# Kernel optimization log

Hardware: AMD Instinct MI355X
Metric: run time of the kernel (lower is better)

## Reference

```python
import jax, jax.numpy as jnp
import numpy as np

DIM = 2048
HEADS = 16
DIM_HEAD = 128
DIM_INNER = HEADS * DIM_HEAD
BATCH = 2
SEQ = 2048
EPS = 1e-12  # F.normalize default eps


def l2norm(t, axis=-1):
    # matches F.normalize(t, dim=axis, p=2): t / max(||t||, eps)
    n = jnp.sqrt(jnp.sum(t * t, axis=axis, keepdims=True))
    return t / jnp.maximum(n, EPS)


def setup_inputs() -> dict:
    key = jax.random.key(0)
    ks = jax.random.split(key, 5)
    x = jax.random.normal(ks[0], (BATCH, SEQ, DIM), dtype=jnp.float32)
    # NormLinear weights (torch Linear layout: [out, in]); parametrization
    # l2-normalizes rows (dim=-1) for q/k/v and columns (dim=0) for to_out.
    Wq = jax.random.normal(ks[1], (DIM_INNER, DIM), dtype=jnp.float32) / np.sqrt(DIM)
    Wk = jax.random.normal(ks[2], (DIM_INNER, DIM), dtype=jnp.float32) / np.sqrt(DIM)
    Wv = jax.random.normal(ks[3], (DIM_INNER, DIM), dtype=jnp.float32) / np.sqrt(DIM)
    Wout = jax.random.normal(ks[4], (DIM, DIM_INNER), dtype=jnp.float32) / np.sqrt(DIM_INNER)
    # Scale(dim_inner, init=1.0, scale=dim**-1): param = ones * dim**-1,
    # forward_scale = init/scale = dim, so qk_scale() starts at 1.0
    qk_scale = jnp.ones((DIM_INNER,), dtype=jnp.float32) / DIM
    return {"x": x, "Wq": Wq, "Wk": Wk, "Wv": Wv, "Wout": Wout, "qk_scale": qk_scale}


def reference(x, Wq, Wk, Wv, Wout, qk_scale):
    b, n, _ = x.shape
    # NormLinear: x @ l2norm(W, rows).T  (scale = groups**-1 = 1)
    q = jnp.einsum('bnd,ed->bne', x, l2norm(Wq, axis=-1))
    k = jnp.einsum('bnd,ed->bne', x, l2norm(Wk, axis=-1))
    v = jnp.einsum('bnd,ed->bne', x, l2norm(Wv, axis=-1))
    # split heads: b n (h d) -> b h n d
    split = lambda t: t.reshape(b, n, HEADS, DIM_HEAD).transpose(0, 2, 1, 3)
    q, k, v = split(q), split(k), split(v)
    # per-head l2norm of q and k over head dim
    q = l2norm(q, axis=-1)
    k = l2norm(k, axis=-1)
    # learned qk scale: (h d) -> h 1 d, effective = param * forward_scale(=DIM)
    q = q * (qk_scale * DIM).reshape(HEADS, 1, DIM_HEAD)
    # causal SDPA with scale = sqrt(dim_head) (unit-norm q,k in nGPT)
    attn_scale = DIM_HEAD ** 0.5
    scores = jnp.einsum('bhid,bhjd->bhij', q, k) * attn_scale
    causal = jnp.tril(jnp.ones((n, n), dtype=bool))
    scores = jnp.where(causal, scores, jnp.finfo(scores.dtype).min)
    attn = jax.nn.softmax(scores, axis=-1)
    out = jnp.einsum('bhij,bhjd->bhid', attn, v)
    # merge heads: b h n d -> b n (h d)
    out = out.transpose(0, 2, 1, 3).reshape(b, n, DIM_INNER)
    # to_out: NormLinear with norm over dim=0 of weight [DIM, DIM_INNER]
    out = jnp.einsum('bne,de->bnd', out, l2norm(Wout, axis=0))
    return out
```

## Files before the change

### kernel.cpp

```cpp
#include <hip/hip_runtime.h>


typedef __bf16 bf16x8 __attribute__((ext_vector_type(8)));
typedef float f32x4 __attribute__((ext_vector_type(4)));

__device__ __forceinline__ unsigned short f2bf(float f) {
  unsigned int u = __float_as_uint(f);
  u = u + 0x7FFFu + ((u >> 16) & 1u);
  return (unsigned short)(u >> 16);
}

__device__ __forceinline__ void async16(const void* g, void* l) {
  __builtin_amdgcn_global_load_lds(
      (const __attribute__((address_space(1))) unsigned int*)g,
      (__attribute__((address_space(3))) unsigned int*)l, 16, 0, 0);
}

#define QFOLD (2048.0f * 11.313708498984761f * 1.4426950408889634f)

__global__ __launch_bounds__(256) void prep_all(
    const float* __restrict__ x, const float* __restrict__ Wq,
    const float* __restrict__ Wk, const float* __restrict__ Wv,
    const float* __restrict__ qks, ushort* __restrict__ xbf,
    ushort* __restrict__ wqn, ushort* __restrict__ wkn,
    ushort* __restrict__ wvn, float* __restrict__ colss,
    float* __restrict__ mh) {
  const int bid = blockIdx.x;
  const int t = threadIdx.x;
  if (bid < 6144) {
    const int z = bid >> 11, row = bid & 2047;
    const float* W = (z == 0) ? Wq : (z == 1) ? Wk : Wv;
    ushort* O = (z == 0) ? wqn : (z == 1) ? wkn : wvn;
    const float4* Wr = (const float4*)(W + (size_t)row * 2048);
    float4 v0 = Wr[t];
    float4 v1 = Wr[t + 256];
    float ss = v0.x * v0.x + v0.y * v0.y + v0.z * v0.z + v0.w * v0.w +
               v1.x * v1.x + v1.y * v1.y + v1.z * v1.z + v1.w * v1.w;
    ss += __shfl_xor(ss, 1);  ss += __shfl_xor(ss, 2);
    ss += __shfl_xor(ss, 4);  ss += __shfl_xor(ss, 8);
    ss += __shfl_xor(ss, 16); ss += __shfl_xor(ss, 32);
    __shared__ float red[4];
    if ((t & 63) == 0) red[t >> 6] = ss;
    __syncthreads();
    float tot = red[0] + red[1] + red[2] + red[3];
    float sc = 1.0f / fmaxf(sqrtf(tot), 1e-12f);
    ushort4 o0, o1;
    o0.x = f2bf(v0.x * sc); o0.y = f2bf(v0.y * sc);
    o0.z = f2bf(v0.z * sc); o0.w = f2bf(v0.w * sc);
    o1.x = f2bf(v1.x * sc); o1.y = f2bf(v1.y * sc);
    o1.z = f2bf(v1.z * sc); o1.w = f2bf(v1.w * sc);
    *(ushort4*)(O + (size_t)row * 2048 + t * 4) = o0;
    *(ushort4*)(O + (size_t)row * 2048 + 1024 + t * 4) = o1;
  } else if (bid < 14336) {
    const int idx = ((bid - 6144) * 256 + t) * 4;
    float4 v = *(const float4*)(x + idx);
    ushort4 o;
    o.x = f2bf(v.x); o.y = f2bf(v.y); o.z = f2bf(v.z); o.w = f2bf(v.w);
    *(ushort4*)(xbf + idx) = o;
  } else if (bid < 14352) {
    const int h = bid - 14336;
    if (t < 64) {
      const int l = t;
      float m = fmaxf(fabsf(qks[h * 128 + l]), fabsf(qks[h * 128 + 64 + l]));
      m = fmaxf(m, __shfl_xor(m, 1));  m = fmaxf(m, __shfl_xor(m, 2));
      m = fmaxf(m, __shfl_xor(m, 4));  m = fmaxf(m, __shfl_xor(m, 8));
      m = fmaxf(m, __shfl_xor(m, 16)); m = fmaxf(m, __shfl_xor(m, 32));
      if (l == 0) mh[h] = m * QFOLD;
    }
  } else {
    float4 z4 = (float4){0.f, 0.f, 0.f, 0.f};
    ((float4*)colss)[t] = z4;
    ((float4*)colss)[t + 256] = z4;
  }
}

__global__ __launch_bounds__(256) void wout_colss(const float* __restrict__ W,
                                                  float* __restrict__ colss) {
  const int e = blockIdx.x * 256 + threadIdx.x;
  const int d0 = blockIdx.y * 128;
  float ss = 0.f;
  #pragma unroll 8
  for (int i = 0; i < 128; ++i) {
    float v = W[(size_t)(d0 + i) * 2048 + e];
    ss += v * v;
  }
  atomicAdd(colss + e, ss);
}

__global__ __launch_bounds__(256) void wout_norm(const float* __restrict__ W,
                                                 const float* __restrict__ colss,
                                                 ushort* __restrict__ O) {
  const int idx = (blockIdx.x * 256 + threadIdx.x) * 4;
  float4 v = *(const float4*)(W + idx);
  float4 c = *(const float4*)(colss + (idx & 2047));
  ushort4 o;
  o.x = f2bf(v.x / fmaxf(sqrtf(c.x), 1e-12f));
  o.y = f2bf(v.y / fmaxf(sqrtf(c.y), 1e-12f));
  o.z = f2bf(v.z / fmaxf(sqrtf(c.z), 1e-12f));
  o.w = f2bf(v.w / fmaxf(sqrtf(c.w), 1e-12f));
  *(ushort4*)(O + idx) = o;
}

__global__ __launch_bounds__(256, 2) void gemm_qkv_fused(
    const ushort* __restrict__ X, const ushort* __restrict__ Wq,
    const ushort* __restrict__ Wk, const ushort* __restrict__ Wv,
    const float* __restrict__ qks, ushort* __restrict__ qn,
    ushort* __restrict__ kn, ushort* __restrict__ vt) {
  const int n0 = blockIdx.x * 128;
  const int m0 = blockIdx.y * 128;
  __shared__ __align__(16) char lds[4 * 16384];
  __shared__ float partials[2][128];
  const int t = threadIdx.x, w = t >> 6, l = t & 63;
  const int wm = w & 1, wn = w >> 1;
  const int l15 = l & 15, l4 = l >> 4;

  f32x4 acc[3][4][4];
  #pragma unroll
  for (int z = 0; z < 3; ++z)
    #pragma unroll
    for (int i = 0; i < 4; ++i)
      #pragma unroll
      for (int j = 0; j < 4; ++j) acc[z][i][j] = (f32x4){0.f, 0.f, 0.f, 0.f};

  const int lc = (t & 7) ^ ((t >> 3) & 7);
  const size_t soff = (size_t)(t >> 3) * 2048 + lc * 8;
  const ushort* sA = X + (size_t)m0 * 2048 + soff;
  const ushort* sQ = Wq + (size_t)n0 * 2048 + soff;
  const ushort* sK = Wk + (size_t)n0 * 2048 + soff;
  const ushort* sV = Wv + (size_t)n0 * 2048 + soff;
  char* dst = lds + t * 16;

  const int rdA = (wm * 64 + l15) * 128;
  const int rdB = (wn * 64 + l15) * 128;
  const int cb0 = (l4 ^ (l15 & 7)) * 16;
  const int cb1 = ((4 + l4) ^ (l15 & 7)) * 16;

  for (int kt = 0; kt < 32; ++kt) {
    const int k0 = kt * 64;
    __syncthreads();
    #pragma unroll
    for (int o = 0; o < 4; ++o) {
      async16(sA + o * 65536 + k0, dst + o * 4096);
      async16(sQ + o * 65536 + k0, dst + 16384 + o * 4096);
      async16(sK + o * 65536 + k0, dst + 32768 + o * 4096);
      async16(sV + o * 65536 + k0, dst + 49152 + o * 4096);
    }
    __syncthreads();
    #pragma unroll
    for (int ks = 0; ks < 2; ++ks) {
      const int cb = ks ? cb1 : cb0;
      bf16x8 af[4];
      #pragma unroll
      for (int f = 0; f < 4; ++f)
        af[f] = *(const bf16x8*)(lds + rdA + f * 2048 + cb);
      #pragma unroll
      for (int z = 0; z < 3; ++z) {
        const char* Bb = lds + 16384 * (1 + z);
        bf16x8 bg[4];
        #pragma unroll
        for (int f = 0; f < 4; ++f)
          bg[f] = *(const bf16x8*)(Bb + rdB + f * 2048 + cb);
        #pragma unroll
        for (int fm = 0; fm < 4; ++fm)
          #pragma unroll
          for (int fn = 0; fn < 4; ++fn)
            acc[z][fm][fn] = __builtin_amdgcn_mfma_f32_16x16x32_bf16(
                af[fm], bg[fn], acc[z][fm][fn], 0, 0, 0);
      }
    }
  }

  const int h = n0 >> 7;

  #pragma unroll
  for (int fm = 0; fm < 4; ++fm) {
    int mrow = m0 + wm * 64 + fm * 16 + l4 * 4;
    int bb = mrow >> 11;
    int nn = mrow & 2047;
    #pragma unroll
    for (int fn = 0; fn < 4; ++fn) {
      int d = wn * 64 + fn * 16 + l15;
      ushort4 p;
      p.x = f2bf(acc[2][fm][fn][0]); p.y = f2bf(acc[2][fm][fn][1]);
      p.z = f2bf(acc[2][fm][fn][2]); p.w = f2bf(acc[2][fm][fn][3]);
      *(ushort4*)(vt + (size_t)((bb * 16 + h) * 128 + d) * 2048 + nn) = p;
    }
  }

  #pragma unroll
  for (int z = 0; z < 2; ++z) {
    __syncthreads();
    float rs[4][4];
    #pragma unroll
    for (int fm = 0; fm < 4; ++fm)
      #pragma unroll
      for (int r = 0; r < 4; ++r) {
        float s = 0.f;
        #pragma unroll
        for (int fn = 0; fn < 4; ++fn) {
          float v = acc[z][fm][fn][r];
          s += v * v;
        }
        s += __shfl_xor(s, 1); s += __shfl_xor(s, 2);
        s += __shfl_xor(s, 4); s += __shfl_xor(s, 8);
        rs[fm][r] = s;
      }
    if (l15 == 0) {
      #pragma unroll
      for (int fm = 0; fm < 4; ++fm)
        #pragma unroll
        for (int r = 0; r < 4; ++r)
          partials[wn][wm * 64 + fm * 16 + l4 * 4 + r] = rs[fm][r];
    }
    __syncthreads();
    float cs[4];
    #pragma unroll
    for (int fn = 0; fn < 4; ++fn)
      cs[fn] = (z == 0) ? qks[n0 + wn * 64 + fn * 16 + l15] * QFOLD : 1.0f;
    ushort* O = (z == 0) ? qn : kn;
    #pragma unroll
    for (int fm = 0; fm < 4; ++fm)
      #pragma unroll
      for (int r = 0; r < 4; ++r) {
        int i = wm * 64 + fm * 16 + l4 * 4 + r;
        float tot = partials[0][i] + partials[1][i];
        float sc = 1.0f / fmaxf(sqrtf(tot), 1e-12f);
        #pragma unroll
        for (int fn = 0; fn < 4; ++fn)
          O[(size_t)(m0 + i) * 2048 + n0 + wn * 64 + fn * 16 + l15] =
              f2bf(acc[z][fm][fn][r] * sc * cs[fn]);
      }
  }
}


#define LDSBUF 49152
#define ABYTES 32768

__device__ __forceinline__ void mainloop_256x128(
    const ushort* __restrict__ A, const ushort* __restrict__ Bw,
    int m0, int n0, char* lds, f32x4 acc[4][4], int t) {
  const int l = t & 63, w = t >> 6;
  const int wm = w & 3, wn = w >> 2;
  const int l15 = l & 15, l4 = l >> 4;

  const int lc = (t & 7) ^ ((t >> 3) & 7);
  const ushort* srcA = A + (size_t)m0 * 2048 + (t >> 3) * 2048 + lc * 8;
  const ushort* srcB = Bw + (size_t)n0 * 2048 + (t >> 3) * 2048 + lc * 8;
  char* dstA = lds + t * 16;
  char* dstB = lds + ABYTES + t * 16;

  const int rdA = (wm * 64 + l15) * 128;
  const int rdB = ABYTES + (wn * 64 + l15) * 128;
  const int cb0 = ((l4 ^ (l15 & 7)) * 16);
  const int cb1 = (((4 + l4) ^ (l15 & 7)) * 16);

  auto stageA = [&](int s, int k0, int o) {
    async16(srcA + (size_t)o * 131072 + k0, dstA + s * LDSBUF + o * 8192);
  };
  auto stageB = [&](int s, int k0, int o) {
    async16(srcB + (size_t)o * 131072 + k0, dstB + s * LDSBUF + o * 8192);
  };

  #pragma unroll
  for (int i = 0; i < 4; ++i)
    #pragma unroll
    for (int j = 0; j < 4; ++j) acc[i][j] = (f32x4){0.f, 0.f, 0.f, 0.f};

  stageA(0, 0, 0); stageA(0, 0, 1); stageA(0, 0, 2); stageA(0, 0, 3);
  stageB(0, 0, 0); stageB(0, 0, 1);
  stageA(1, 64, 0); stageA(1, 64, 1); stageA(1, 64, 2); stageA(1, 64, 3);
  stageB(1, 64, 0); stageB(1, 64, 1);
  asm volatile("s_waitcnt vmcnt(6)" ::: "memory");
  __builtin_amdgcn_s_barrier();

  auto tile = [&](int s, int s2, int k2, bool pf) {
    const char* Ab = lds + s * LDSBUF;
    bf16x8 af[4][2], bg[4][2];
    #pragma unroll
    for (int fm = 0; fm < 4; ++fm) {
      af[fm][0] = *(const bf16x8*)(Ab + rdA + fm * 2048 + cb0);
      af[fm][1] = *(const bf16x8*)(Ab + rdA + fm * 2048 + cb1);
    }
    #pragma unroll
    for (int fn = 0; fn < 2; ++fn) {
      bg[fn][0] = *(const bf16x8*)(Ab + rdB + fn * 2048 + cb0);
      bg[fn][1] = *(const bf16x8*)(Ab + rdB + fn * 2048 + cb1);
    }
    if (pf) { stageA(s2, k2, 0); stageA(s2, k2, 1); stageA(s2, k2, 2); }
    __builtin_amdgcn_s_setprio(1);
    #pragma unroll
    for (int ks = 0; ks < 2; ++ks)
      #pragma unroll
      for (int fm = 0; fm < 4; ++fm)
        #pragma unroll
        for (int fn = 0; fn < 2; ++fn)
          acc[fm][fn] = __builtin_amdgcn_mfma_f32_16x16x32_bf16(
              af[fm][ks], bg[fn][ks], acc[fm][fn], 0, 0, 0);
    __builtin_amdgcn_s_setprio(0);
    #pragma unroll
    for (int fn = 2; fn < 4; ++fn) {
      bg[fn][0] = *(const bf16x8*)(Ab + rdB + fn * 2048 + cb0);
      bg[fn][1] = *(const bf16x8*)(Ab + rdB + fn * 2048 + cb1);
    }
    if (pf) { stageA(s2, k2, 3); stageB(s2, k2, 0); stageB(s2, k2, 1); }
    __builtin_amdgcn_s_setprio(1);
    #pragma unroll
    for (int ks = 0; ks < 2; ++ks)
      #pragma unroll
      for (int fm = 0; fm < 4; ++fm)
        #pragma unroll
        for (int fn = 2; fn < 4; ++fn)
          acc[fm][fn] = __builtin_amdgcn_mfma_f32_16x16x32_bf16(
              af[fm][ks], bg[fn][ks], acc[fm][fn], 0, 0, 0);
    __builtin_amdgcn_s_setprio(0);
  };

  #pragma unroll 1
  for (int kt = 0; kt < 30; kt += 3) {
    tile(0, 2, (kt + 2) * 64, true);
    asm volatile("s_waitcnt vmcnt(6)" ::: "memory");
    __builtin_amdgcn_s_barrier();
    tile(1, 0, (kt + 3) * 64, true);
    asm volatile("s_waitcnt vmcnt(6)" ::: "memory");
    __builtin_amdgcn_s_barrier();
    tile(2, 1, (kt + 4) * 64, true);
    asm volatile("s_waitcnt vmcnt(6)" ::: "memory");
    __builtin_amdgcn_s_barrier();
  }
  tile(0, 0, 0, false);
  asm volatile("s_waitcnt vmcnt(0)" ::: "memory");
  __builtin_amdgcn_s_barrier();
  tile(1, 0, 0, false);
}

__global__ __launch_bounds__(256, 3) void attn_kernel(
    const ushort* __restrict__ qn, const ushort* __restrict__ kn,
    const ushort* __restrict__ vt, const float* __restrict__ mhead,
    ushort* __restrict__ ao) {
  const int hb = blockIdx.x;
  const int b = hb >> 4, h = hb & 15;
  const int qt = 31 - blockIdx.y;
  const int i0 = qt * 64;
  const int t = threadIdx.x, w = t >> 6, l = t & 63;
  const int l15 = l & 15, l4 = l >> 4;

  __shared__ __align__(16) ushort Ks[64 * 136];
  __shared__ __align__(16) ushort Vts[128 * 72];
  __shared__ __align__(16) ushort Ps[64 * 72];

  bf16x8 qf[4];
  #pragma unroll
  for (int ks = 0; ks < 4; ++ks)
    qf[ks] = *(const bf16x8*)(qn +
        (size_t)(b * 2048 + i0 + w * 16 + l15) * 2048 +
        h * 128 + ks * 32 + l4 * 8);

  f32x4 Oa[8];
  #pragma unroll
  for (int fd = 0; fd < 8; ++fd) Oa[fd] = (f32x4){0.f, 0.f, 0.f, 0.f};
  f32x4 Ol = (f32x4){0.f, 0.f, 0.f, 0.f};

  const float mh = mhead[h];
  const __bf16 one = (__bf16)1.0f;
  const bf16x8 ones = {one, one, one, one, one, one, one, one};

  const ushort* kbase = kn + (size_t)(b * 2048) * 2048 + h * 128;
  const ushort* vbase = vt + (size_t)((b * 16 + h) * 128) * 2048;

  for (int jt = 0; jt <= qt; ++jt) {
    const int j0 = jt * 64;
    __syncthreads();
    #pragma unroll
    for (int pass = 0; pass < 5; ++pass) {
      int c = pass * 256 + t;
      if (c < 1088) {
        int r = c / 17, dc = c - r * 17;
        int dcc = (dc == 16) ? 0 : dc;
        async16(kbase + (size_t)(j0 + r) * 2048 + dcc * 8, (char*)Ks + c * 16);
      }
    }
    #pragma unroll
    for (int pass = 0; pass < 5; ++pass) {
      int c = pass * 256 + t;
      if (c < 1152) {
        int r = c / 9, jc = c - r * 9;
        int jcc = (jc == 8) ? 0 : jc;
        async16(vbase + (size_t)r * 2048 + j0 + jcc * 8, (char*)Vts + c * 16);
      }
    }
    __syncthreads();

    f32x4 Sa[4];
    #pragma unroll
    for (int fj = 0; fj < 4; ++fj) {
      f32x4 s0 = (f32x4){0.f, 0.f, 0.f, 0.f};
      #pragma unroll
      for (int ks = 0; ks < 4; ++ks) {
        bf16x8 kf = *(const bf16x8*)&Ks[(fj * 16 + l15) * 136 + ks * 32 + l4 * 8];
        s0 = __builtin_amdgcn_mfma_f32_16x16x32_bf16(qf[ks], kf, s0, 0, 0, 0);
      }
      Sa[fj] = s0;
    }

    if (jt == qt) {
      #pragma unroll
      for (int fj = 0; fj < 4; ++fj)
        #pragma unroll
        for (int r = 0; r < 4; ++r) {
          int jg = fj * 16 + l15;
          int ig = w * 16 + l4 * 4 + r;
          if (jg > ig) Sa[fj][r] = -1e30f;
        }
    }

    #pragma unroll
    for (int fj = 0; fj < 4; ++fj)
      #pragma unroll
      for (int r = 0; r < 4; ++r)
        Ps[(w * 16 + l4 * 4 + r) * 72 + fj * 16 + l15] =
            f2bf(__builtin_exp2f(Sa[fj][r] - mh));

    #pragma unroll
    for (int ks = 0; ks < 2; ++ks) {
      bf16x8 p0 = *(const bf16x8*)&Ps[(w * 16 + l15) * 72 + ks * 32 + l4 * 8];
      Ol = __builtin_amdgcn_mfma_f32_16x16x32_bf16(p0, ones, Ol, 0, 0, 0);
      #pragma unroll
      for (int fd = 0; fd < 8; ++fd) {
        bf16x8 vf = *(const bf16x8*)&Vts[(fd * 16 + l15) * 72 + ks * 32 + l4 * 8];
        Oa[fd] = __builtin_amdgcn_mfma_f32_16x16x32_bf16(p0, vf, Oa[fd], 0, 0, 0);
      }
    }
  }

  #pragma unroll
  for (int r = 0; r < 4; ++r) {
    float inv = 1.0f / Ol[r];
    int ig = i0 + w * 16 + l4 * 4 + r;
    #pragma unroll
    for (int fd = 0; fd < 8; ++fd)
      ao[(size_t)(b * 2048 + ig) * 2048 + h * 128 + fd * 16 + l15] =
          f2bf(Oa[fd][r] * inv);
  }
}

__global__ __launch_bounds__(512, 2) void gemm_out(
    const ushort* __restrict__ A, const ushort* __restrict__ Bw,
    float* __restrict__ C) {
  __shared__ __align__(16) char lds[3 * LDSBUF];
  const int n0 = blockIdx.x * 128;
  const int m0 = blockIdx.y * 256;
  const int t = threadIdx.x;
  const int l = t & 63, w = t >> 6;
  const int wm = w & 3, wn = w >> 2;
  const int l15 = l & 15, l4 = l >> 4;

  f32x4 acc[4][4];
  mainloop_256x128(A, Bw, m0, n0, lds, acc, t);

  #pragma unroll
  for (int fm = 0; fm < 4; ++fm)
    #pragma unroll
    for (int fn = 0; fn < 4; ++fn)
      #pragma unroll
      for (int r = 0; r < 4; ++r)
        C[(size_t)(m0 + wm * 64 + fm * 16 + l4 * 4 + r) * 2048 +
          n0 + wn * 64 + fn * 16 + l15] = acc[fm][fn][r];
}

extern "C" void kernel_launch(void* const* d_in, const int* in_sizes, int n_in,
                              void* d_out, int out_size, void* d_ws, size_t ws_size,
                              hipStream_t stream) {
  (void)in_sizes; (void)n_in; (void)out_size; (void)ws_size;
  const float* x    = (const float*)d_in[0];
  const float* Wq   = (const float*)d_in[1];
  const float* Wk   = (const float*)d_in[2];
  const float* Wv   = (const float*)d_in[3];
  const float* Wout = (const float*)d_in[4];
  const float* qks  = (const float*)d_in[5];
  char* ws = (char*)d_ws;

  ushort* wqn  = (ushort*)(ws + 0);
  ushort* wkn  = (ushort*)(ws + 8388608);
  ushort* wvn  = (ushort*)(ws + 16777216);
  ushort* wotn = (ushort*)(ws + 25165824);
  ushort* xbf  = (ushort*)(ws + 33554432);
  ushort* qn   = (ushort*)(ws + 50331648);
  ushort* kn   = (ushort*)(ws + 67108864);
  ushort* vt   = (ushort*)(ws + 83886080);
  ushort* ao   = (ushort*)(ws + 100663296);
  float* colss = (float*)(ws + 117440512);
  float* mh    = (float*)(ws + 117448704);
  float* out   = (float*)d_out;

  prep_all<<<14353, 256, 0, stream>>>(x, Wq, Wk, Wv, qks, xbf, wqn, wkn, wvn,
                                      colss, mh);
  wout_colss<<<dim3(8, 16), 256, 0, stream>>>(Wout, colss);
  wout_norm<<<4096, 256, 0, stream>>>(Wout, colss, wotn);
  gemm_qkv_fused<<<dim3(16, 32), 256, 0, stream>>>(xbf, wqn, wkn, wvn, qks,
                                                   qn, kn, vt);
  attn_kernel<<<dim3(32, 32), 256, 0, stream>>>(qn, kn, vt, mh, ao);
  gemm_out<<<dim3(16, 16), 512, 0, stream>>>(ao, wotn, out);
}
```

Before: 338.0 us.

## Double-buffer QKV GEMM LDS staging with K=32 tiles and async prefetch

Restructures the fused QKV projection GEMM mainloop from a single-buffered K=64 tile to a double-buffered K=32 pipeline. Global-to-LDS loads for tile kt+2 are issued while computing on the current buffer, with explicit vmcnt waits and raw barriers in place of __syncthreads. The LDS layout packs X/Wq and Wk/Wv halves into shared 16 KB regions within the same LDS footprint. It also raises wave priority around the MFMA blocks. This aims to hide global load latency behind MFMA work, at the cost of twice as many barriers per K and some fragility in the manual waitcnt accounting.

```diff
diff --git a/kernel.cpp b/kernel.cpp
--- a/kernel.cpp
+++ b/kernel.cpp
@@ -108,7 +108,7 @@
     ushort* __restrict__ kn, ushort* __restrict__ vt) {
   const int n0 = blockIdx.x * 128;
   const int m0 = blockIdx.y * 128;
-  __shared__ __align__(16) char lds[4 * 16384];
+  __shared__ __align__(16) char lds[2 * 32768];
   __shared__ float partials[2][128];
   const int t = threadIdx.x, w = t >> 6, l = t & 63;
   const int wm = w & 1, wn = w >> 1;
@@ -122,53 +122,74 @@
       #pragma unroll
       for (int j = 0; j < 4; ++j) acc[z][i][j] = (f32x4){0.f, 0.f, 0.f, 0.f};
 
-  const int lc = (t & 7) ^ ((t >> 3) & 7);
-  const size_t soff = (size_t)(t >> 3) * 2048 + lc * 8;
-  const ushort* sA = X + (size_t)m0 * 2048 + soff;
-  const ushort* sQ = Wq + (size_t)n0 * 2048 + soff;
-  const ushort* sK = Wk + (size_t)n0 * 2048 + soff;
-  const ushort* sV = Wv + (size_t)n0 * 2048 + soff;
-  char* dst = lds + t * 16;
-
+  const int srow = t >> 3;
+  const int lg = (t & 7) ^ (srow & 7);
+  const ushort* sAQ = (lg < 4)
+      ? X  + (size_t)(m0 + srow) * 2048 + lg * 8
+      : Wq + (size_t)(n0 + srow) * 2048 + (lg - 4) * 8;
+  const ushort* sKV = (lg < 4)
+      ? Wk + (size_t)(n0 + srow) * 2048 + lg * 8
+      : Wv + (size_t)(n0 + srow) * 2048 + (lg - 4) * 8;
+  char* dAQ = lds + t * 16;
+  char* dKV = lds + 16384 + t * 16;
+
+  auto stage = [&](int buf, int kt) {
+    const int k0 = kt * 32;
+    #pragma unroll
+    for (int o = 0; o < 4; ++o) {
+      async16(sAQ + (size_t)o * 65536 + k0, dAQ + buf * 32768 + o * 4096);
+      async16(sKV + (size_t)o * 65536 + k0, dKV + buf * 32768 + o * 4096);
+    }
+  };
+
+  const int rsw = l15 & 7;
   const int rdA = (wm * 64 + l15) * 128;
   const int rdB = (wn * 64 + l15) * 128;
-  const int cb0 = (l4 ^ (l15 & 7)) * 16;
-  const int cb1 = ((4 + l4) ^ (l15 & 7)) * 16;
-
-  for (int kt = 0; kt < 32; ++kt) {
-    const int k0 = kt * 64;
-    __syncthreads();
-    #pragma unroll
-    for (int o = 0; o < 4; ++o) {
-      async16(sA + o * 65536 + k0, dst + o * 4096);
-      async16(sQ + o * 65536 + k0, dst + 16384 + o * 4096);
-      async16(sK + o * 65536 + k0, dst + 32768 + o * 4096);
-      async16(sV + o * 65536 + k0, dst + 49152 + o * 4096);
-    }
-    __syncthreads();
-    #pragma unroll
-    for (int ks = 0; ks < 2; ++ks) {
-      const int cb = ks ? cb1 : cb0;
-      bf16x8 af[4];
+  const int cLo = (l4 ^ rsw) * 16;
+  const int cHi = ((4 + l4) ^ rsw) * 16;
+
+  auto tile = [&](const char* base) {
+    const char* AQ = base;
+    const char* KV = base + 16384;
+    bf16x8 af[4], bg[4];
+    #pragma unroll
+    for (int f = 0; f < 4; ++f)
+      af[f] = *(const bf16x8*)(AQ + rdA + f * 2048 + cLo);
+    #pragma unroll
+    for (int z = 0; z < 3; ++z) {
       #pragma unroll
       for (int f = 0; f < 4; ++f)
-        af[f] = *(const bf16x8*)(lds + rdA + f * 2048 + cb);
-      #pragma unroll
-      for (int z = 0; z < 3; ++z) {
-        const char* Bb = lds + 16384 * (1 + z);
-        bf16x8 bg[4];
-        #pragma unroll
-        for (int f = 0; f < 4; ++f)
-          bg[f] = *(const bf16x8*)(Bb + rdB + f * 2048 + cb);
-        #pragma unroll
-        for (int fm = 0; fm < 4; ++fm)
-          #pragma unroll
-          for (int fn = 0; fn < 4; ++fn)
-            acc[z][fm][fn] = __builtin_amdgcn_mfma_f32_16x16x32_bf16(
-                af[fm], bg[fn], acc[z][fm][fn], 0, 0, 0);
-      }
-    }
-  }
+        bg[f] = (z == 0) ? *(const bf16x8*)(AQ + rdB + f * 2048 + cHi)
+              : (z == 1) ? *(const bf16x8*)(KV + rdB + f * 2048 + cLo)
+                         : *(const bf16x8*)(KV + rdB + f * 2048 + cHi);
+      __builtin_amdgcn_s_setprio(1);
+      #pragma unroll
+      for (int fm = 0; fm < 4; ++fm)
+        #pragma unroll
+        for (int fn = 0; fn < 4; ++fn)
+          acc[z][fm][fn] = __builtin_amdgcn_mfma_f32_16x16x32_bf16(
+              af[fm], bg[fn], acc[z][fm][fn], 0, 0, 0);
+      __builtin_amdgcn_s_setprio(0);
+    }
+  };
+
+  stage(0, 0);
+  stage(1, 1);
+  asm volatile("s_waitcnt vmcnt(8)" ::: "memory");
+  __builtin_amdgcn_s_barrier();
+
+  #pragma unroll 2
+  for (int kt = 0; kt < 62; ++kt) {
+    tile(lds + (kt & 1) * 32768);
+    __builtin_amdgcn_s_barrier();
+    stage(kt & 1, kt + 2);
+    asm volatile("s_waitcnt vmcnt(8)" ::: "memory");
+    __builtin_amdgcn_s_barrier();
+  }
+  tile(lds);
+  asm volatile("s_waitcnt vmcnt(0)" ::: "memory");
+  __builtin_amdgcn_s_barrier();
+  tile(lds + 32768);
 
   const int h = n0 >> 7;
 
```

Measured after the change: 366.6 us. 8.5% more time.
